# Performance work log

Measured on AMD Instinct MI355X. Metric: run time of the kernel, lower is better.

## Reference

```python
import jax, jax.numpy as jnp
import numpy as np

N = 25000        # nodes
E = 400000       # edges (avg degree 16)
F = 128          # num_features
NRBF = 20        # num_rbf_features
CUTOFF = 5.0


def setup_inputs() -> dict:
    key = jax.random.key(0)
    ks = jax.random.split(key, 9)
    node_scalar = jax.random.normal(ks[0], (N, F), jnp.float32)
    node_vector = jax.random.normal(ks[1], (N, F, 3), jnp.float32)
    dst = jax.random.randint(ks[2], (E,), 0, N)
    src = jax.random.randint(ks[3], (E,), 0, N)
    r = jax.random.normal(ks[4], (E, 3), jnp.float32) * 1.5
    d = jnp.clip(jnp.linalg.norm(r, axis=-1), 0.1, None)
    adj_matrix = jnp.concatenate(
        [dst[:, None].astype(jnp.float32), src[:, None].astype(jnp.float32), r, d[:, None]],
        axis=-1)  # [E, 6]
    s_in = 1.0 / np.sqrt(F)
    s_rbf = 1.0 / np.sqrt(NRBF)
    W1 = jax.random.normal(ks[5], (F, F), jnp.float32) * s_in
    b1 = jnp.zeros((F,), jnp.float32)
    W2 = jax.random.normal(ks[6], (F, 3 * F), jnp.float32) * s_in
    b2 = jnp.zeros((3 * F,), jnp.float32)
    Wr = jax.random.normal(ks[7], (NRBF, 3 * F), jnp.float32) * s_rbf
    br = jnp.zeros((3 * F,), jnp.float32)
    return dict(node_scalar=node_scalar, node_vector=node_vector, adj_matrix=adj_matrix,
                W1=W1, b1=b1, W2=W2, b2=b2, Wr=Wr, br=br)


def reference(node_scalar, node_vector, adj_matrix, W1, b1, W2, b2, Wr, br):
    # scalar message MLP: Linear -> SiLU -> Linear, [N, 3F]
    atom_scalar = jax.nn.silu(node_scalar @ W1 + b1) @ W2 + b2

    dst = adj_matrix[:, 0].astype(jnp.int32)
    src = adj_matrix[:, 1].astype(jnp.int32)
    r_ij = adj_matrix[:, 2:5]              # [E, 3]
    d = adj_matrix[:, 5]                   # [E]

    # sinc expansion: sin(d * n * pi / cutoff) / d, n = 1..NRBF -> [E, NRBF]
    n_vals = jnp.arange(1, NRBF + 1, dtype=jnp.float32)
    sinc = jnp.sin(d[:, None] * n_vals * jnp.pi / CUTOFF) / d[:, None]
    rbf = sinc @ Wr + br                   # [E, 3F]
    cut = jnp.where(d < CUTOFF, 0.5 * (jnp.cos(jnp.pi * d / CUTOFF) + 1.0), 0.0)
    w = rbf * cut[:, None]                 # [E, 3F]

    pre_split = atom_scalar[src] * w       # [E, 3F]
    s1, s2, s3 = jnp.split(pre_split, 3, axis=-1)  # each [E, F]

    r_hat = r_ij / d[:, None]              # [E, 3]
    # message_vector: [E, F, 3]
    message_vector = node_vector[src] * s1[:, :, None] + s3[:, :, None] * r_hat[:, None, :]

    delta_s = jnp.zeros_like(node_scalar).at[dst].add(s2)
    delta_v = jnp.zeros_like(node_vector).at[dst].add(message_vector)
    return node_scalar + delta_s, node_vector + delta_v
```

## Files before the change

kernel.cpp:

```cpp
#include <hip/hip_runtime.h>

#define FDIM 128
#define NRBF 20
constexpr float CUTOFF_F = 5.0f;
constexpr float PI_F = 3.14159265358979323846f;

typedef _Float16 h2 __attribute__((ext_vector_type(2)));
typedef _Float16 half4 __attribute__((ext_vector_type(4)));
typedef float f32x4 __attribute__((ext_vector_type(4)));

__device__ __forceinline__ uint packh(float a, float b) {
  union { _Float16 h[2]; uint u; } x;
  x.h[0] = (_Float16)a;
  x.h[1] = (_Float16)b;
  return x.u;
}
__device__ __forceinline__ float h_lo(uint w) {
  union { uint u; _Float16 h[2]; } x;
  x.u = w;
  return (float)x.h[0];
}
__device__ __forceinline__ float h_hi(uint w) {
  union { uint u; _Float16 h[2]; } x;
  x.u = w;
  return (float)x.h[1];
}
__device__ __forceinline__ float dot2(uint cw, h2 w, float acc) {
#if __has_builtin(__builtin_amdgcn_fdot2)
  h2 c = __builtin_bit_cast(h2, cw);
  return __builtin_amdgcn_fdot2(c, w, acc, false);
#else
  return fmaf(h_hi(cw), (float)w[1], fmaf(h_lo(cw), (float)w[0], acc));
#endif
}

__global__ __launch_bounds__(256) void wconv2(const float* __restrict__ W1,
                                              const float* __restrict__ W2,
                                              _Float16* __restrict__ w1h,
                                              _Float16* __restrict__ w2h,
                                              int* __restrict__ counts,
                                              int Ncnt) {
  int idx = blockIdx.x * blockDim.x + threadIdx.x;
  if (idx < Ncnt) counts[idx] = 0;
  const float* W;
  _Float16* outp;
  int NC, NCOLS, base;
  if (idx < 8 * 8 * 256) {
    W = W1; outp = w1h; NC = 8; NCOLS = 128; base = idx;
  } else if (idx < 8 * 8 * 256 + 8 * 24 * 256) {
    W = W2; outp = w2h; NC = 24; NCOLS = 384; base = idx - 8 * 8 * 256;
  } else {
    return;
  }
  int i = base & 3;
  int l = (base >> 2) & 63;
  int rem = base >> 8;
  int c = rem % NC, s = rem / NC;
  int k = s * 16 + ((l >> 4) & 3) * 4 + i;
  int col = c * 16 + (l & 15);
  outp[base] = (_Float16)W[(size_t)k * NCOLS + col];
}

__global__ __launch_bounds__(256) void hist_kernel(const float* __restrict__ adj,
                                                   int* __restrict__ counts,
                                                   int E) {
  int e = blockIdx.x * blockDim.x + threadIdx.x;
  if (e < E) atomicAdd(&counts[(int)adj[(size_t)e * 6]], 1);
}

__global__ __launch_bounds__(1024) void scan_kernel(
    const int* __restrict__ counts, int* __restrict__ offs,
    int* __restrict__ cursor, int n) {
  __shared__ int part[1024];
  const int tid = threadIdx.x;
  const int CH = (n + 1023) >> 10;
  const int b = tid * CH;
  const int e = min(b + CH, n);
  int s = 0;
  for (int i = b; i < e; ++i) s += counts[i];
  part[tid] = s;
  __syncthreads();
  for (int off = 1; off < 1024; off <<= 1) {
    int v = (tid >= off) ? part[tid - off] : 0;
    __syncthreads();
    part[tid] += v;
    __syncthreads();
  }
  int run = part[tid] - s;
  if (tid == 0) offs[0] = 0;
  for (int i = b; i < e; ++i) {
    int c = counts[i];
    cursor[i] = run;
    run += c;
    offs[i + 1] = run;
  }
}

__global__ __launch_bounds__(256) void prep_gemm(
    const float* __restrict__ A, const half4* __restrict__ w1h,
    const float* __restrict__ b1, const half4* __restrict__ w2h,
    const float* __restrict__ b2, const float* __restrict__ nvec,
    uint* __restrict__ bundle, int M, const float* __restrict__ adj,
    int* __restrict__ cursor, int* __restrict__ eids, uint* __restrict__ rec,
    int E, int GB) {
  __shared__ _Float16 Ah[64][136];
  const int t = threadIdx.x;

  if ((int)blockIdx.x >= GB) {
    int e = ((int)blockIdx.x - GB) * 256 + t;
    if (e >= E) return;
    const float* a = adj + (size_t)e * 6;
    int dst = (int)a[0];
    int src = (int)a[1];
    float rx = a[2], ry = a[3], rz = a[4], d = a[5];

    int p = atomicAdd(&cursor[dst], 1);
    eids[p] = e;

    float x = d * (PI_F / CUTOFF_F);
    float sx, cx;
    __sincosf(x, &sx, &cx);
    float invd = 1.f / d;
    float cut = (d < CUTOFF_F) ? 0.5f * (cx + 1.f) : 0.f;
    float sc = invd * cut;

    union { uint w[14]; uint2 q[7]; } R;
    R.w[0] = (uint)src;
    R.w[1] = packh(rx * invd, ry * invd);
    R.w[2] = packh(rz * invd, cut);
    float twoc = 2.f * cx;
    float sprev = 0.f, scur = sx;
    float c[NRBF];
#pragma unroll
    for (int n = 0; n < NRBF; ++n) {
      c[n] = scur * sc;
      float nxt = fmaf(twoc, scur, -sprev);
      sprev = scur;
      scur = nxt;
    }
#pragma unroll
    for (int m = 0; m < 10; ++m) R.w[3 + m] = packh(c[2 * m], c[2 * m + 1]);
    R.w[13] = 0;
    uint2* o = (uint2*)(rec + (size_t)p * 14);
#pragma unroll
    for (int m = 0; m < 7; ++m) o[m] = R.q[m];
    return;
  }

  const int w = t >> 6;
  const int l = t & 63;
  const int lr = l & 15, lg = (l >> 4) & 3;
  const int row0 = blockIdx.x * 64;

  for (int i = t; i < 64 * 32; i += 256) {
    int r = i >> 5, c4 = (i & 31) << 2;
    int gr = row0 + r;
    float4 v = make_float4(0.f, 0.f, 0.f, 0.f);
    if (gr < M) v = *(const float4*)&A[(size_t)gr * FDIM + c4];
    half4 hv = {(_Float16)v.x, (_Float16)v.y, (_Float16)v.z, (_Float16)v.w};
    *(half4*)&Ah[r][c4] = hv;
  }
  __syncthreads();

  half4 af[8];
#pragma unroll
  for (int s = 0; s < 8; ++s)
    af[s] = *(const half4*)&Ah[16 * w + lr][s * 16 + lg * 4];

  f32x4 acc1[8];
#pragma unroll
  for (int c = 0; c < 8; ++c) acc1[c] = {0.f, 0.f, 0.f, 0.f};
#pragma unroll
  for (int s = 0; s < 8; ++s) {
#pragma unroll
    for (int c = 0; c < 8; ++c) {
      half4 bf = w1h[(s * 8 + c) * 64 + l];
      acc1[c] = __builtin_amdgcn_mfma_f32_16x16x16f16(af[s], bf, acc1[c], 0, 0, 0);
    }
  }
  __syncthreads();
#pragma unroll
  for (int c = 0; c < 8; ++c) {
    float bb = b1[c * 16 + lr];
#pragma unroll
    for (int r = 0; r < 4; ++r) {
      float x = acc1[c][r] + bb;
      x = x / (1.f + __expf(-x));
      Ah[16 * w + lg * 4 + r][c * 16 + lr] = (_Float16)x;
    }
  }
  __syncthreads();

  half4 hf[8];
#pragma unroll
  for (int s = 0; s < 8; ++s)
    hf[s] = *(const half4*)&Ah[16 * w + lr][s * 16 + lg * 4];

#pragma unroll 1
  for (int cg = 0; cg < 8; ++cg) {
    f32x4 a3[3];
#pragma unroll
    for (int p = 0; p < 3; ++p) a3[p] = {0.f, 0.f, 0.f, 0.f};
#pragma unroll
    for (int s = 0; s < 8; ++s) {
#pragma unroll
      for (int p = 0; p < 3; ++p) {
        half4 bf = w2h[(s * 24 + cg + p * 8) * 64 + l];
        a3[p] = __builtin_amdgcn_mfma_f32_16x16x16f16(hf[s], bf, a3[p], 0, 0, 0);
      }
    }
    const int j = cg * 16 + lr;
    const float bb0 = b2[j], bb1 = b2[j + 128], bb2 = b2[j + 256];
#pragma unroll
    for (int r = 0; r < 4; ++r) {
      int n = row0 + 16 * w + lg * 4 + r;
      if (n >= M) continue;
      const float* vb = nvec + ((size_t)n * FDIM + j) * 3;
      float v0 = vb[0], v1 = vb[1], v2 = vb[2];
      uint* o = bundle + ((size_t)n * FDIM + j) * 3;
      o[0] = packh(a3[0][r] + bb0, a3[1][r] + bb1);
      o[1] = packh(a3[2][r] + bb2, v0);
      o[2] = packh(v1, v2);
    }
  }
}

__global__ __launch_bounds__(128) void accum_kernel(
    const uint* __restrict__ rec, const uint* __restrict__ bundle,
    const float* __restrict__ nvec, const float* __restrict__ Wr,
    const float* __restrict__ br, const float* __restrict__ ns,
    const int* __restrict__ offs, const int* __restrict__ eids,
    float* __restrict__ out_s, float* __restrict__ out_v, int Nn) {
  const int j = threadIdx.x;

  h2 wp0[10], wp1[10], wp2[10];
#pragma unroll
  for (int m = 0; m < 10; ++m) {
    wp0[m] = h2{(_Float16)Wr[(2 * m) * 384 + j], (_Float16)Wr[(2 * m + 1) * 384 + j]};
    wp1[m] = h2{(_Float16)Wr[(2 * m) * 384 + 128 + j], (_Float16)Wr[(2 * m + 1) * 384 + 128 + j]};
    wp2[m] = h2{(_Float16)Wr[(2 * m) * 384 + 256 + j], (_Float16)Wr[(2 * m + 1) * 384 + 256 + j]};
  }
  const float brj0 = br[j], brj1 = br[j + 128], brj2 = br[j + 256];

  __shared__ int sh_e[128], sh_pos[128];

#define SLOT(t) ((t) < 128 ? sh_pos[(t)] : (t))
#define LOADREC(R, t)                                                      \
  {                                                                        \
    int su = __builtin_amdgcn_readfirstlane(beg + SLOT(t));                \
    const uint* p = rec + (size_t)(uint)su * 14;                           \
    _Pragma("unroll") for (int w_ = 0; w_ < 13; ++w_) R[w_] = p[w_];       \
  }
#define LOADB(B0, B1, B2, SRC)                                             \
  {                                                                        \
    const uint* p = bundle + ((size_t)(uint)(SRC)*FDIM + j) * 3;           \
    B0 = p[0];                                                             \
    B1 = p[1];                                                             \
    B2 = p[2];                                                             \
  }

  for (int d = blockIdx.x; d < Nn; d += gridDim.x) {
    const int beg = offs[d];
    const int cnt = offs[d + 1] - beg;
    const int m = cnt < 128 ? cnt : 128;
    if (j < m) sh_e[j] = eids[beg + j];
    __syncthreads();
    if (j < m) {
      int v = sh_e[j];
      int r = 0;
      for (int u = 0; u < m; ++u) r += (sh_e[u] < v);
      sh_pos[r] = j;
    }
    __syncthreads();

    float acc_s = 0.f, av0 = 0.f, av1 = 0.f, av2 = 0.f;

    uint r_cur[13], r_nxt[13];
    uint b0 = 0, b1 = 0, b2 = 0;
    if (cnt > 0) LOADREC(r_cur, 0);
    if (cnt > 1) LOADREC(r_nxt, 1);
    if (cnt > 0) LOADB(b0, b1, b2, (int)r_cur[0]);

    for (int t = 0; t < cnt; ++t) {
      uint nb0 = 0, nb1 = 0, nb2 = 0;
      if (t + 1 < cnt) LOADB(nb0, nb1, nb2, (int)r_nxt[0]);
      uint r_n2[13];
      if (t + 2 < cnt) LOADREC(r_n2, t + 2);

      float rhx = h_lo(r_cur[1]), rhy = h_hi(r_cur[1]);
      float rhz = h_lo(r_cur[2]), cut = h_hi(r_cur[2]);
      float w0 = cut * brj0, w1 = cut * brj1, w2 = cut * brj2;
#pragma unroll
      for (int q = 0; q < 10; ++q) {
        w0 = dot2(r_cur[3 + q], wp0[q], w0);
        w1 = dot2(r_cur[3 + q], wp1[q], w1);
        w2 = dot2(r_cur[3 + q], wp2[q], w2);
      }
      float s1 = h_lo(b0) * w0;
      float s2 = h_hi(b0) * w1;
      float s3 = h_lo(b1) * w2;
      float pv0 = h_hi(b1), pv1 = h_lo(b2), pv2 = h_hi(b2);
      acc_s += s2;
      av0 = fmaf(pv0, s1, fmaf(s3, rhx, av0));
      av1 = fmaf(pv1, s1, fmaf(s3, rhy, av1));
      av2 = fmaf(pv2, s1, fmaf(s3, rhz, av2));

#pragma unroll
      for (int w_ = 0; w_ < 13; ++w_) {
        r_cur[w_] = r_nxt[w_];
        r_nxt[w_] = r_n2[w_];
      }
      b0 = nb0;
      b1 = nb1;
      b2 = nb2;
    }

    out_s[(size_t)d * FDIM + j] = ns[(size_t)d * FDIM + j] + acc_s;
    float* vo = out_v + (size_t)d * 384 + j * 3;
    const float* vi = nvec + (size_t)d * 384 + j * 3;
    vo[0] = vi[0] + av0;
    vo[1] = vi[1] + av1;
    vo[2] = vi[2] + av2;
  }
#undef SLOT
#undef LOADREC
#undef LOADB
}

extern "C" void kernel_launch(void* const* d_in, const int* in_sizes, int n_in,
                              void* d_out, int out_size, void* d_ws,
                              size_t ws_size, hipStream_t stream) {
  const float* node_scalar = (const float*)d_in[0];
  const float* node_vector = (const float*)d_in[1];
  const float* adj = (const float*)d_in[2];
  const float* W1 = (const float*)d_in[3];
  const float* b1 = (const float*)d_in[4];
  const float* W2 = (const float*)d_in[5];
  const float* b2 = (const float*)d_in[6];
  const float* Wr = (const float*)d_in[7];
  const float* br = (const float*)d_in[8];

  const int N = in_sizes[0] / FDIM;
  const int E = in_sizes[2] / 6;

  float* out = (float*)d_out;
  float* out_s = out;
  float* out_v = out + (size_t)N * FDIM;

  char* w = (char*)d_ws;
  uint* bundle = (uint*)w;
  size_t off = (size_t)N * FDIM * 12;
  uint* rec = (uint*)(w + off);
  off += (size_t)E * 56;
  _Float16* w1h = (_Float16*)(w + off);
  off += 8 * 8 * 256 * 2;
  _Float16* w2h = (_Float16*)(w + off);
  off += 8 * 24 * 256 * 2;
  int* counts = (int*)(w + off);
  int* offs = counts + N;
  int* cursor = offs + N + 1;
  int* eids = cursor + N;

  wconv2<<<(8 * 8 * 256 + 8 * 24 * 256 + 255) / 256, 256, 0, stream>>>(
      W1, W2, w1h, w2h, counts, N);
  hist_kernel<<<(E + 255) / 256, 256, 0, stream>>>(adj, counts, E);
  scan_kernel<<<1, 1024, 0, stream>>>(counts, offs, cursor, N);

  const int GB = (N + 63) / 64;
  const int EB = (E + 255) / 256;
  prep_gemm<<<GB + EB, 256, 0, stream>>>(node_scalar, (const half4*)w1h, b1,
                                         (const half4*)w2h, b2, node_vector,
                                         bundle, N, adj, cursor, eids, rec, E,
                                         GB);

  const int agrid = N < 4096 ? N : 4096;
  accum_kernel<<<agrid, 128, 0, stream>>>(rec, bundle, node_vector, Wr, br,
                                          node_scalar, offs, eids, out_s,
                                          out_v, N);
}
```

Measured before the change: 273.8 us.

## Process two destination nodes per block iteration to interleave edge streams

The accumulation kernel now handles a pair of destination nodes per loop iteration, running two independent prefetch and compute pipelines side by side. The aim is more memory-level parallelism per wave, so the gather latency of one node's edges overlaps with the other's. In exchange it roughly doubles register use for record buffers, which may lower occupancy, and it adds divergence when the two nodes have different degrees. The grid is halved to match.

```diff
diff --git a/kernel.cpp b/kernel.cpp
--- a/kernel.cpp
+++ b/kernel.cpp
@@ -242,12 +242,12 @@
   }
   const float brj0 = br[j], brj1 = br[j + 128], brj2 = br[j + 256];
 
-  __shared__ int sh_e[128], sh_pos[128];
-
-#define SLOT(t) ((t) < 128 ? sh_pos[(t)] : (t))
-#define LOADREC(R, t)                                                      \
+  __shared__ int sh_e[2][128], sh_pos[2][128];
+
+#define SLOT(S, t) ((t) < 128 ? sh_pos[S][(t)] : (t))
+#define LOADREC(R, S, BEG, t)                                              \
   {                                                                        \
-    int su = __builtin_amdgcn_readfirstlane(beg + SLOT(t));                \
+    int su = __builtin_amdgcn_readfirstlane((BEG) + SLOT(S, t));           \
     const uint* p = rec + (size_t)(uint)su * 14;                           \
     _Pragma("unroll") for (int w_ = 0; w_ < 13; ++w_) R[w_] = p[w_];       \
   }
@@ -258,73 +258,112 @@
     B1 = p[1];                                                             \
     B2 = p[2];                                                             \
   }
-
-  for (int d = blockIdx.x; d < Nn; d += gridDim.x) {
-    const int beg = offs[d];
-    const int cnt = offs[d + 1] - beg;
-    const int m = cnt < 128 ? cnt : 128;
-    if (j < m) sh_e[j] = eids[beg + j];
+#define COMPUTE(RC, B0, B1, B2, ACC, AV0, AV1, AV2)                        \
+  {                                                                        \
+    float rhx = h_lo(RC[1]), rhy = h_hi(RC[1]);                            \
+    float rhz = h_lo(RC[2]), cut = h_hi(RC[2]);                            \
+    float w0 = cut * brj0, w1 = cut * brj1, w2 = cut * brj2;               \
+    _Pragma("unroll") for (int q = 0; q < 10; ++q) {                       \
+      w0 = dot2(RC[3 + q], wp0[q], w0);                                    \
+      w1 = dot2(RC[3 + q], wp1[q], w1);                                    \
+      w2 = dot2(RC[3 + q], wp2[q], w2);                                    \
+    }                                                                      \
+    float s1 = h_lo(B0) * w0;                                              \
+    float s2 = h_hi(B0) * w1;                                              \
+    float s3 = h_lo(B1) * w2;                                              \
+    float pv0 = h_hi(B1), pv1 = h_lo(B2), pv2 = h_hi(B2);                  \
+    ACC += s2;                                                             \
+    AV0 = fmaf(pv0, s1, fmaf(s3, rhx, AV0));                               \
+    AV1 = fmaf(pv1, s1, fmaf(s3, rhy, AV1));                               \
+    AV2 = fmaf(pv2, s1, fmaf(s3, rhz, AV2));                               \
+  }
+
+  const int nPairs = (Nn + 1) >> 1;
+  for (int pr = blockIdx.x; pr < nPairs; pr += gridDim.x) {
+    const int dA = pr * 2;
+    const int dB = dA + 1;
+    const int begA = offs[dA];
+    const int cntA = offs[dA + 1] - begA;
+    int begB = 0, cntB = 0;
+    if (dB < Nn) {
+      begB = offs[dB];
+      cntB = offs[dB + 1] - begB;
+    }
+    const int mA = cntA < 128 ? cntA : 128;
+    const int mB = cntB < 128 ? cntB : 128;
+    if (j < mA) sh_e[0][j] = eids[begA + j];
+    if (j < mB) sh_e[1][j] = eids[begB + j];
     __syncthreads();
-    if (j < m) {
-      int v = sh_e[j];
+    if (j < mA) {
+      int v = sh_e[0][j];
       int r = 0;
-      for (int u = 0; u < m; ++u) r += (sh_e[u] < v);
-      sh_pos[r] = j;
+      for (int u = 0; u < mA; ++u) r += (sh_e[0][u] < v);
+      sh_pos[0][r] = j;
+    }
+    if (j < mB) {
+      int v = sh_e[1][j];
+      int r = 0;
+      for (int u = 0; u < mB; ++u) r += (sh_e[1][u] < v);
+      sh_pos[1][r] = j;
     }
     __syncthreads();
 
-    float acc_s = 0.f, av0 = 0.f, av1 = 0.f, av2 = 0.f;
-
-    uint r_cur[13], r_nxt[13];
-    uint b0 = 0, b1 = 0, b2 = 0;
-    if (cnt > 0) LOADREC(r_cur, 0);
-    if (cnt > 1) LOADREC(r_nxt, 1);
-    if (cnt > 0) LOADB(b0, b1, b2, (int)r_cur[0]);
-
-    for (int t = 0; t < cnt; ++t) {
-      uint nb0 = 0, nb1 = 0, nb2 = 0;
-      if (t + 1 < cnt) LOADB(nb0, nb1, nb2, (int)r_nxt[0]);
-      uint r_n2[13];
-      if (t + 2 < cnt) LOADREC(r_n2, t + 2);
-
-      float rhx = h_lo(r_cur[1]), rhy = h_hi(r_cur[1]);
-      float rhz = h_lo(r_cur[2]), cut = h_hi(r_cur[2]);
-      float w0 = cut * brj0, w1 = cut * brj1, w2 = cut * brj2;
-#pragma unroll
-      for (int q = 0; q < 10; ++q) {
-        w0 = dot2(r_cur[3 + q], wp0[q], w0);
-        w1 = dot2(r_cur[3 + q], wp1[q], w1);
-        w2 = dot2(r_cur[3 + q], wp2[q], w2);
+    float accA = 0.f, avA0 = 0.f, avA1 = 0.f, avA2 = 0.f;
+    float accB = 0.f, avB0 = 0.f, avB1 = 0.f, avB2 = 0.f;
+
+    uint rA0[13], rA1[13], rB0[13], rB1[13];
+    uint bA0 = 0, bA1 = 0, bA2 = 0, bB0 = 0, bB1 = 0, bB2 = 0;
+    if (cntA > 0) LOADREC(rA0, 0, begA, 0);
+    if (cntB > 0) LOADREC(rB0, 1, begB, 0);
+    if (cntA > 1) LOADREC(rA1, 0, begA, 1);
+    if (cntB > 1) LOADREC(rB1, 1, begB, 1);
+    if (cntA > 0) LOADB(bA0, bA1, bA2, (int)rA0[0]);
+    if (cntB > 0) LOADB(bB0, bB1, bB2, (int)rB0[0]);
+
+    const int tmax = cntA > cntB ? cntA : cntB;
+    for (int t = 0; t < tmax; ++t) {
+      uint nA0 = 0, nA1 = 0, nA2 = 0, nB0 = 0, nB1 = 0, nB2 = 0;
+      if (t + 1 < cntA) LOADB(nA0, nA1, nA2, (int)rA1[0]);
+      if (t + 1 < cntB) LOADB(nB0, nB1, nB2, (int)rB1[0]);
+      uint rA2[13], rB2[13];
+      if (t + 2 < cntA) LOADREC(rA2, 0, begA, t + 2);
+      if (t + 2 < cntB) LOADREC(rB2, 1, begB, t + 2);
+
+      if (t < cntA) COMPUTE(rA0, bA0, bA1, bA2, accA, avA0, avA1, avA2);
+      if (t < cntB) COMPUTE(rB0, bB0, bB1, bB2, accB, avB0, avB1, avB2);
+
+#pragma unroll
+      for (int w_ = 0; w_ < 13; ++w_) {
+        rA0[w_] = rA1[w_];
+        rA1[w_] = rA2[w_];
+        rB0[w_] = rB1[w_];
+        rB1[w_] = rB2[w_];
       }
-      float s1 = h_lo(b0) * w0;
-      float s2 = h_hi(b0) * w1;
-      float s3 = h_lo(b1) * w2;
-      float pv0 = h_hi(b1), pv1 = h_lo(b2), pv2 = h_hi(b2);
-      acc_s += s2;
-      av0 = fmaf(pv0, s1, fmaf(s3, rhx, av0));
-      av1 = fmaf(pv1, s1, fmaf(s3, rhy, av1));
-      av2 = fmaf(pv2, s1, fmaf(s3, rhz, av2));
-
-#pragma unroll
-      for (int w_ = 0; w_ < 13; ++w_) {
-        r_cur[w_] = r_nxt[w_];
-        r_nxt[w_] = r_n2[w_];
-      }
-      b0 = nb0;
-      b1 = nb1;
-      b2 = nb2;
-    }
-
-    out_s[(size_t)d * FDIM + j] = ns[(size_t)d * FDIM + j] + acc_s;
-    float* vo = out_v + (size_t)d * 384 + j * 3;
-    const float* vi = nvec + (size_t)d * 384 + j * 3;
-    vo[0] = vi[0] + av0;
-    vo[1] = vi[1] + av1;
-    vo[2] = vi[2] + av2;
+      bA0 = nA0; bA1 = nA1; bA2 = nA2;
+      bB0 = nB0; bB1 = nB1; bB2 = nB2;
+    }
+
+    out_s[(size_t)dA * FDIM + j] = ns[(size_t)dA * FDIM + j] + accA;
+    {
+      float* vo = out_v + (size_t)dA * 384 + j * 3;
+      const float* vi = nvec + (size_t)dA * 384 + j * 3;
+      vo[0] = vi[0] + avA0;
+      vo[1] = vi[1] + avA1;
+      vo[2] = vi[2] + avA2;
+    }
+    if (dB < Nn) {
+      out_s[(size_t)dB * FDIM + j] = ns[(size_t)dB * FDIM + j] + accB;
+      float* vo = out_v + (size_t)dB * 384 + j * 3;
+      const float* vi = nvec + (size_t)dB * 384 + j * 3;
+      vo[0] = vi[0] + avB0;
+      vo[1] = vi[1] + avB1;
+      vo[2] = vi[2] + avB2;
+    }
   }
 #undef SLOT
 #undef LOADREC
 #undef LOADB
+#undef COMPUTE
 }
 
 extern "C" void kernel_launch(void* const* d_in, const int* in_sizes, int n_in,
@@ -373,7 +412,8 @@
                                          bundle, N, adj, cursor, eids, rec, E,
                                          GB);
 
-  const int agrid = N < 4096 ? N : 4096;
+  const int nPairs = (N + 1) / 2;
+  const int agrid = nPairs < 4096 ? nPairs : 4096;
   accum_kernel<<<agrid, 128, 0, stream>>>(rec, bundle, node_vector, Wr, br,
                                           node_scalar, offs, eids, out_s,
                                           out_v, N);
```

Result: slower. 437.1 us (+59.6%).
